# Optimization experiments

Measured on AMD Instinct MI355X. Metric: run time of the kernel, lower is better.

## Reference

```python
import jax, jax.numpy as jnp
import numpy as np

N_GENE = 4762
N_CELL = 847


def _graph_conv(x_src, src, dst, n_src, n_dst, W, b):
    """DGL GraphConv with norm='both': D_src^{-1/2} A D_dst^{-1/2} X W + b."""
    ones_e = jnp.ones(src.shape, jnp.float32)
    deg_out = jax.ops.segment_sum(ones_e, src, num_segments=n_src)
    norm_src = jnp.clip(deg_out, 1.0, None) ** -0.5
    feat = x_src * norm_src[:, None]            # [n_src, d]
    msg = feat[src]                              # gather  [E, d]
    agg = jax.ops.segment_sum(msg, dst, num_segments=n_dst)  # scatter-add [n_dst, d]
    deg_in = jax.ops.segment_sum(ones_e, dst, num_segments=n_dst)
    norm_dst = jnp.clip(deg_in, 1.0, None) ** -0.5
    return (agg * norm_dst[:, None]) @ W + b


def setup_inputs() -> dict:
    key = jax.random.key(0)
    ks = jax.random.split(key, 12)
    E = 200000
    d = 256
    inp = {
        "gene_emb": jax.random.normal(ks[0], (N_GENE, d), jnp.float32),
        "cell_emb": jax.random.normal(ks[1], (N_CELL, d), jnp.float32),
        "W_g2c": jax.random.normal(ks[2], (d, d), jnp.float32) * (1.0 / np.sqrt(d)),
        "b_g2c": jnp.zeros((d,), jnp.float32),
        "W_c2g": jax.random.normal(ks[3], (d, d), jnp.float32) * (1.0 / np.sqrt(d)),
        "b_c2g": jnp.zeros((d,), jnp.float32),
        "Wp": jax.random.normal(ks[4], (2 * d, 1), jnp.float32) * (1.0 / np.sqrt(2 * d)),
        "bp": jnp.zeros((1,), jnp.float32),
        "g2c_src": jax.random.randint(ks[5], (E,), 0, N_GENE, jnp.int32),
        "g2c_dst": jax.random.randint(ks[6], (E,), 0, N_CELL, jnp.int32),
        "c2g_src": jax.random.randint(ks[7], (E,), 0, N_CELL, jnp.int32),
        "c2g_dst": jax.random.randint(ks[8], (E,), 0, N_GENE, jnp.int32),
        "dec_src": jax.random.randint(ks[9], (E,), 0, N_GENE, jnp.int32),
        "dec_dst": jax.random.randint(ks[10], (E,), 0, N_CELL, jnp.int32),
    }
    return inp


def reference(gene_emb, cell_emb, W_g2c, b_g2c, W_c2g, b_c2g, Wp, bp,
              g2c_src, g2c_dst, c2g_src, c2g_dst, dec_src, dec_dst):
    # HeteroGraphConv (aggregate='sum'): each dst type receives from one relation here.
    h_cell = _graph_conv(gene_emb, g2c_src, g2c_dst, N_GENE, N_CELL, W_g2c, b_g2c)
    h_gene = _graph_conv(cell_emb, c2g_src, c2g_dst, N_CELL, N_GENE, W_c2g, b_c2g)
    h_gene = jax.nn.relu(h_gene)
    h_cell = jax.nn.relu(h_cell)
    # HeteroMLPPredictor: concat(src_h, dst_h) @ Wp + bp on dec_graph edges.
    x = jnp.concatenate([h_gene[dec_src], h_cell[dec_dst]], axis=1)  # [E_dec, 512]
    score = x @ Wp + bp                                               # [E_dec, 1]
    return (score, h_gene, h_cell)
```

## Files before the change

kernel.cpp:

```cpp
#include <hip/hip_runtime.h>

#define N_GENE 4762
#define N_CELL 847
#define NEDGE  200000
#define D      256
#define NPART  64

typedef __attribute__((ext_vector_type(8))) short short8;
typedef __attribute__((ext_vector_type(8))) unsigned short ushort8v;
typedef __attribute__((ext_vector_type(4))) float f32x4;

#define S_G_OUT 0
#define S_C_IN  (S_G_OUT + N_GENE)
#define S_C_OUT (S_C_IN + N_CELL)
#define S_G_IN  (S_C_OUT + N_CELL)
#define NBINS   (S_G_IN + N_GENE)

#define ALIGN8(x) (((x) + 7) & ~7)

#define A_DEG      0
#define A_NRM      (A_DEG + NBINS)
#define A_OFFS_C   (A_NRM + NBINS)
#define A_OFFS_G   (A_OFFS_C + N_CELL + 1)
#define A_SORT_C   ALIGN8(A_OFFS_G + N_GENE + 1)
#define A_SORT_G   (A_SORT_C + 2 * NEDGE)
#define A_PART     (A_SORT_G + 2 * NEDGE)
#define A_SG       (A_PART + NPART * NBINS)
#define A_SC       (A_SG + N_GENE)
#define A_GENE_BF  ALIGN8(A_SC + N_CELL)
#define A_CELL_BF  ALIGN8(A_GENE_BF + N_GENE * D / 2)
#define A_WT1_BF   ALIGN8(A_CELL_BF + N_CELL * D / 2)
#define A_WT2_BF   ALIGN8(A_WT1_BF + D * D / 2)
#define A_AGGC_BF  ALIGN8(A_WT2_BF + D * D / 2)
#define A_AGGG_BF  ALIGN8(A_AGGC_BF + N_CELL * D / 2)

__device__ __forceinline__ unsigned short f2bf(float f) {
    unsigned u = __float_as_uint(f);
    u = (u + 0x7FFFu + ((u >> 16) & 1u)) >> 16;
    return (unsigned short)u;
}
__device__ __forceinline__ float bf2f(unsigned short b) {
    return __uint_as_float(((unsigned)b) << 16);
}

__global__ __launch_bounds__(1024) void k_pre(
        const int* __restrict__ g2c_src, const int* __restrict__ g2c_dst,
        const int* __restrict__ c2g_src, const int* __restrict__ c2g_dst,
        const float* __restrict__ gene_emb, const float* __restrict__ cell_emb,
        const float* __restrict__ W_g2c, const float* __restrict__ W_c2g,
        int* __restrict__ partial,
        unsigned short* __restrict__ gene_bf, unsigned short* __restrict__ cell_bf,
        unsigned short* __restrict__ wt1, unsigned short* __restrict__ wt2) {
    __shared__ int sh[NBINS];
    int B = blockIdx.x, T = threadIdx.x;
    if (B < NPART) {
        for (int j = T; j < NBINS; j += 1024) sh[j] = 0;
        __syncthreads();
        const int chunk = (NEDGE + NPART - 1) / NPART;
        int e0 = B * chunk, e1 = min(NEDGE, e0 + chunk);
        for (int e = e0 + T; e < e1; e += 1024) {
            atomicAdd(&sh[S_G_OUT + g2c_src[e]], 1);
            atomicAdd(&sh[S_C_IN  + g2c_dst[e]], 1);
            atomicAdd(&sh[S_C_OUT + c2g_src[e]], 1);
            atomicAdd(&sh[S_G_IN  + c2g_dst[e]], 1);
        }
        __syncthreads();
        int* pp = partial + B * NBINS;
        for (int j = T; j < NBINS; j += 1024) pp[j] = sh[j];
    } else {
        const int NG = N_GENE * D, NC = N_CELL * D, NW = D * D;
        const int total = NG + NC + 2 * NW;
        for (int i = (B - NPART) * 1024 + T; i < total; i += NPART * 1024) {
            if (i < NG) {
                gene_bf[i] = f2bf(gene_emb[i]);
            } else if (i < NG + NC) {
                int j = i - NG;
                cell_bf[j] = f2bf(cell_emb[j]);
            } else if (i < NG + NC + NW) {
                int j = i - NG - NC;
                wt1[j] = f2bf(W_g2c[(j & 255) * D + (j >> 8)]);
            } else {
                int j = i - NG - NC - NW;
                wt2[j] = f2bf(W_c2g[(j & 255) * D + (j >> 8)]);
            }
        }
    }
}

__global__ void k_reduce(int* __restrict__ partial, int* __restrict__ deg,
                         float* __restrict__ nrm) {
    int j = blockIdx.x * blockDim.x + threadIdx.x;
    if (j < NBINS) {
        int s = 0;
        #pragma unroll
        for (int b0 = 0; b0 < NPART; b0 += 32) {
            int t[32];
            #pragma unroll
            for (int u = 0; u < 32; u++) t[u] = partial[(b0 + u) * NBINS + j];
            #pragma unroll
            for (int u = 0; u < 32; u++) { partial[(b0 + u) * NBINS + j] = s; s += t[u]; }
        }
        deg[j] = s;
        nrm[j] = rsqrtf(fmaxf((float)s, 1.0f));
    }
}

__global__ __launch_bounds__(1024) void k_scatter(
        const int* __restrict__ g2c_src, const int* __restrict__ g2c_dst,
        const int* __restrict__ c2g_src, const int* __restrict__ c2g_dst,
        const int* __restrict__ deg, const int* __restrict__ partial,
        const float* __restrict__ nrm,
        int* __restrict__ offsC, int* __restrict__ offsG,
        int2* __restrict__ sortC, int2* __restrict__ sortG) {
    __shared__ int soffs[N_GENE + 1];
    __shared__ int scur[N_GENE];
    __shared__ int wsum[16];
    int T = threadIdx.x, blk = blockIdx.x, dir = blockIdx.y;
    const int* src  = dir ? c2g_src : g2c_src;
    const int* dst  = dir ? c2g_dst : g2c_dst;
    const int* dgs  = dir ? deg + S_G_IN : deg + S_C_IN;
    const float* nsv = dir ? nrm + S_C_OUT : nrm + S_G_OUT;
    int seg         = dir ? S_G_IN : S_C_IN;
    int nb          = dir ? N_GENE : N_CELL;
    int* goffs      = dir ? offsG : offsC;
    int2* sorted    = dir ? sortG : sortC;
    int per = (nb + 1023) >> 10;
    int i0 = T * per, i1 = min(nb, i0 + per);
    int loc[5];
    int s = 0;
    for (int i = i0; i < i1; i++) { loc[i - i0] = s; s += dgs[i]; }
    int lane = T & 63, w = T >> 6;
    int t = s;
    #pragma unroll
    for (int off = 1; off < 64; off <<= 1) {
        int u = __shfl_up(t, off);
        if (lane >= off) t += u;
    }
    if (lane == 63) wsum[w] = t;
    __syncthreads();
    if (w == 0 && lane < 16) {
        int x = wsum[lane];
        #pragma unroll
        for (int off = 1; off < 16; off <<= 1) {
            int u = __shfl_up(x, off);
            if (lane >= off) x += u;
        }
        wsum[lane] = x;
    }
    __syncthreads();
    int wbase = w ? wsum[w - 1] : 0;
    int excl = wbase + t - s;
    for (int i = i0; i < i1; i++) soffs[i] = excl + loc[i - i0];
    if (T == 1023) soffs[nb] = excl + s;
    __syncthreads();
    if (blk == 0)
        for (int j = T; j <= nb; j += 1024) goffs[j] = soffs[j];
    const int* basep = partial + blk * NBINS + seg;
    for (int j = T; j < nb; j += 1024) scur[j] = soffs[j] + basep[j];
    __syncthreads();
    const int chunk = (NEDGE + NPART - 1) / NPART;
    int e0 = blk * chunk, e1 = min(NEDGE, e0 + chunk);
    for (int e = e0 + T; e < e1; e += 1024) {
        int d = dst[e], sv = src[e];
        float nv = nsv[sv];
        int pos = atomicAdd(&scur[d], 1);
        sorted[pos] = make_int2(sv, __float_as_int(nv));
    }
}

__global__ __launch_bounds__(256) void k_agg(
        const unsigned short* __restrict__ gene_bf,
        const unsigned short* __restrict__ cell_bf,
        const int2* __restrict__ sortC, const int2* __restrict__ sortG,
        const int* __restrict__ offsC, const int* __restrict__ offsG,
        const float* __restrict__ nrm,
        unsigned short* __restrict__ aggC, unsigned short* __restrict__ aggG) {
    __shared__ int   sidx[4][64];
    __shared__ float snrm[4][64];
    __shared__ float pacc[4][256];
    int w = threadIdx.x >> 6, lane = threadIdx.x & 63;
    int half = lane >> 5, li = lane & 31;
    int B = blockIdx.x;
    bool isCell = B < N_CELL;

    int e0, e1;
    const unsigned short* emb;
    const int2* sorted;
    int node;
    if (isCell) {
        node = B;
        int f0 = offsC[node], f1 = offsC[node + 1];
        int ne = f1 - f0, nw = (ne + 3) >> 2;
        e0 = f0 + w * nw; e1 = min(f1, e0 + nw);
        emb = gene_bf; sorted = sortC;
    } else {
        node = (B - N_CELL) * 4 + w;
        if (node >= N_GENE) return;
        e0 = offsG[node]; e1 = offsG[node + 1];
        emb = cell_bf; sorted = sortG;
    }

    float acc[8];
    #pragma unroll
    for (int c = 0; c < 8; c++) acc[c] = 0.f;

    for (int base = e0; base < e1; base += 64) {
        int n = min(64, e1 - base);
        if (lane < n) {
            int2 pr = sorted[base + lane];
            sidx[w][lane] = pr.x;
            snrm[w][lane] = __int_as_float(pr.y);
        }
        int i = 0;
        for (; 2 * i + 8 <= n; i += 4) {
            int j0 = 2 * i + half, j1 = 2 * i + 2 + half;
            int j2 = 2 * i + 4 + half, j3 = 2 * i + 6 + half;
            ushort8v v0 = *(const ushort8v*)&emb[sidx[w][j0] * D + li * 8];
            ushort8v v1 = *(const ushort8v*)&emb[sidx[w][j1] * D + li * 8];
            ushort8v v2 = *(const ushort8v*)&emb[sidx[w][j2] * D + li * 8];
            ushort8v v3 = *(const ushort8v*)&emb[sidx[w][j3] * D + li * 8];
            float n0 = snrm[w][j0], n1 = snrm[w][j1];
            float n2 = snrm[w][j2], n3 = snrm[w][j3];
            #pragma unroll
            for (int c = 0; c < 8; c++)
                acc[c] += bf2f(v0[c]) * n0 + bf2f(v1[c]) * n1 +
                          bf2f(v2[c]) * n2 + bf2f(v3[c]) * n3;
        }
        int npair = (n + 1) >> 1;
        for (; i < npair; i++) {
            int jj = 2 * i + half;
            bool ok = jj < n;
            int idx = ok ? sidx[w][jj] : sidx[w][0];
            float nv = ok ? snrm[w][jj] : 0.f;
            ushort8v v = *(const ushort8v*)&emb[idx * D + li * 8];
            #pragma unroll
            for (int c = 0; c < 8; c++) acc[c] += bf2f(v[c]) * nv;
        }
    }
    #pragma unroll
    for (int c = 0; c < 8; c++) acc[c] += __shfl_xor(acc[c], 32);

    if (isCell) {
        if (half == 0) {
            #pragma unroll
            for (int c = 0; c < 8; c++) pacc[w][li * 8 + c] = acc[c];
        }
        __syncthreads();
        int T = threadIdx.x;
        float s2 = pacc[0][T] + pacc[1][T] + pacc[2][T] + pacc[3][T];
        aggC[node * D + T] = f2bf(s2 * nrm[S_C_IN + node]);
    } else {
        if (half == 0) {
            float ndv = nrm[S_G_IN + node];
            ushort8v o;
            #pragma unroll
            for (int c = 0; c < 8; c++) o[c] = f2bf(acc[c] * ndv);
            *(ushort8v*)&aggG[node * D + li * 8] = o;
        }
    }
}

__global__ __launch_bounds__(256) void k_gemm2(
        const unsigned short* __restrict__ aggC, const unsigned short* __restrict__ aggG,
        const unsigned short* __restrict__ wt1, const unsigned short* __restrict__ wt2,
        const float* __restrict__ b_g2c, const float* __restrict__ b_c2g,
        const float* __restrict__ Wp,
        float* __restrict__ hC, float* __restrict__ hG,
        float* __restrict__ sg, float* __restrict__ sc) {
    const int CT = (N_CELL + 15) / 16;
    const int GT = (N_GENE + 15) / 16;
    int wid = blockIdx.x * 4 + (threadIdx.x >> 6);
    if (wid >= CT + GT) return;
    bool isCell = wid < CT;
    int tile = isCell ? wid : wid - CT;
    int m0 = tile * 16;
    int M = isCell ? N_CELL : N_GENE;
    const unsigned short* A  = isCell ? aggC : aggG;
    const unsigned short* Wt = isCell ? wt1 : wt2;
    const float* bias = isCell ? b_g2c : b_c2g;
    const float* wp   = isCell ? Wp + D : Wp;
    float* H  = isCell ? hC : hG;
    float* sv = isCell ? sc : sg;
    int lane = threadIdx.x & 63;
    int l15 = lane & 15, quad = lane >> 4;
    int arow = m0 + l15;
    if (arow >= M) arow = M - 1;
    f32x4 acc[16];
    #pragma unroll
    for (int t = 0; t < 16; t++) acc[t] = (f32x4){0.f, 0.f, 0.f, 0.f};
    #pragma unroll
    for (int k0 = 0; k0 < D; k0 += 32) {
        short8 a = *(const short8*)&A[arow * D + k0 + quad * 8];
        #pragma unroll
        for (int t = 0; t < 16; t++) {
            short8 b = *(const short8*)&Wt[(t * 16 + l15) * D + k0 + quad * 8];
            acc[t] = __builtin_amdgcn_mfma_f32_16x16x32_bf16(a, b, acc[t], 0, 0, 0);
        }
    }
    float dot[4] = {0.f, 0.f, 0.f, 0.f};
    #pragma unroll
    for (int t = 0; t < 16; t++) {
        int col = t * 16 + l15;
        float bv = bias[col], wv = wp[col];
        #pragma unroll
        for (int r = 0; r < 4; r++) {
            int row = m0 + quad * 4 + r;
            float h = fmaxf(acc[t][r] + bv, 0.f);
            if (row < M) H[row * D + col] = h;
            dot[r] += h * wv;
        }
    }
    #pragma unroll
    for (int off = 1; off < 16; off <<= 1) {
        #pragma unroll
        for (int r = 0; r < 4; r++) dot[r] += __shfl_xor(dot[r], off);
    }
    if (l15 == 0) {
        #pragma unroll
        for (int r = 0; r < 4; r++) {
            int row = m0 + quad * 4 + r;
            if (row < M) sv[row] = dot[r];
        }
    }
}

__global__ void k_score(const int* __restrict__ dsrc, const int* __restrict__ ddst,
                        const float* __restrict__ sg, const float* __restrict__ sc,
                        const float* __restrict__ bp, float* __restrict__ out) {
    int i = blockIdx.x * blockDim.x + threadIdx.x;
    if (i < NEDGE) out[i] = sg[dsrc[i]] + sc[ddst[i]] + bp[0];
}

extern "C" void kernel_launch(void* const* d_in, const int* in_sizes, int n_in,
                              void* d_out, int out_size, void* d_ws, size_t ws_size,
                              hipStream_t stream) {
    const float* gene_emb = (const float*)d_in[0];
    const float* cell_emb = (const float*)d_in[1];
    const float* W_g2c    = (const float*)d_in[2];
    const float* b_g2c    = (const float*)d_in[3];
    const float* W_c2g    = (const float*)d_in[4];
    const float* b_c2g    = (const float*)d_in[5];
    const float* Wp       = (const float*)d_in[6];
    const float* bp       = (const float*)d_in[7];
    const int* g2c_src = (const int*)d_in[8];
    const int* g2c_dst = (const int*)d_in[9];
    const int* c2g_src = (const int*)d_in[10];
    const int* c2g_dst = (const int*)d_in[11];
    const int* dec_src = (const int*)d_in[12];
    const int* dec_dst = (const int*)d_in[13];

    int*   wsi = (int*)d_ws;
    float* wsf = (float*)d_ws;
    unsigned short* gene_bf = (unsigned short*)(wsi + A_GENE_BF);
    unsigned short* cell_bf = (unsigned short*)(wsi + A_CELL_BF);
    unsigned short* wt1     = (unsigned short*)(wsi + A_WT1_BF);
    unsigned short* wt2     = (unsigned short*)(wsi + A_WT2_BF);
    unsigned short* aggC    = (unsigned short*)(wsi + A_AGGC_BF);
    unsigned short* aggG    = (unsigned short*)(wsi + A_AGGG_BF);
    int2* sortC = (int2*)(wsi + A_SORT_C);
    int2* sortG = (int2*)(wsi + A_SORT_G);

    float* out = (float*)d_out;
    float* out_score = out;
    float* out_hgene = out + NEDGE;
    float* out_hcell = out + NEDGE + N_GENE * D;

    k_pre<<<2 * NPART, 1024, 0, stream>>>(g2c_src, g2c_dst, c2g_src, c2g_dst,
                                          gene_emb, cell_emb, W_g2c, W_c2g,
                                          wsi + A_PART, gene_bf, cell_bf, wt1, wt2);
    k_reduce<<<(NBINS + 255) / 256, 256, 0, stream>>>(wsi + A_PART, wsi + A_DEG,
                                                      wsf + A_NRM);
    {
        dim3 grid(NPART, 2);
        k_scatter<<<grid, 1024, 0, stream>>>(g2c_src, g2c_dst, c2g_src, c2g_dst,
                                             wsi + A_DEG, wsi + A_PART, wsf + A_NRM,
                                             wsi + A_OFFS_C, wsi + A_OFFS_G,
                                             sortC, sortG);
    }
    k_agg<<<N_CELL + (N_GENE + 3) / 4, 256, 0, stream>>>(
        gene_bf, cell_bf, sortC, sortG, wsi + A_OFFS_C, wsi + A_OFFS_G,
        wsf + A_NRM, aggC, aggG);
    {
        const int CT = (N_CELL + 15) / 16, GT = (N_GENE + 15) / 16;
        k_gemm2<<<(CT + GT + 3) / 4, 256, 0, stream>>>(aggC, aggG, wt1, wt2,
                                                       b_g2c, b_c2g, Wp,
                                                       out_hcell, out_hgene,
                                                       wsf + A_SG, wsf + A_SC);
    }
    k_score<<<(NEDGE + 255) / 256, 256, 0, stream>>>(dec_src, dec_dst,
                                                     wsf + A_SG, wsf + A_SC, bp, out_score);
}
```

Measured before the change: 159.3 us.

## Fold degree reduction into scatter kernel and vectorize bf16 conversion

Removes the separate k_reduce launch. Each scatter block now recomputes degree totals, source norms and its per-block base offsets directly from a transposed partial-histogram layout, and k_agg derives the destination norm from the CSR offsets. The embedding-to-bf16 conversion is vectorized to float4 loads and ushort4 stores. This saves one kernel launch and a global round trip, but every one of the 128 scatter blocks redundantly reads the full partial histogram, adding memory traffic and latency inside the scatter.

```diff
diff --git a/kernel.cpp b/kernel.cpp
--- a/kernel.cpp
+++ b/kernel.cpp
@@ -18,14 +18,12 @@
 
 #define ALIGN8(x) (((x) + 7) & ~7)
 
-#define A_DEG      0
-#define A_NRM      (A_DEG + NBINS)
-#define A_OFFS_C   (A_NRM + NBINS)
+#define A_OFFS_C   0
 #define A_OFFS_G   (A_OFFS_C + N_CELL + 1)
 #define A_SORT_C   ALIGN8(A_OFFS_G + N_GENE + 1)
 #define A_SORT_G   (A_SORT_C + 2 * NEDGE)
 #define A_PART     (A_SORT_G + 2 * NEDGE)
-#define A_SG       (A_PART + NPART * NBINS)
+#define A_SG       (A_PART + NBINS * NPART)
 #define A_SC       (A_SG + N_GENE)
 #define A_GENE_BF  ALIGN8(A_SC + N_CELL)
 #define A_CELL_BF  ALIGN8(A_GENE_BF + N_GENE * D / 2)
@@ -65,70 +63,78 @@
             atomicAdd(&sh[S_G_IN  + c2g_dst[e]], 1);
         }
         __syncthreads();
-        int* pp = partial + B * NBINS;
-        for (int j = T; j < NBINS; j += 1024) pp[j] = sh[j];
+        for (int j = T; j < NBINS; j += 1024) partial[j * NPART + B] = sh[j];
     } else {
-        const int NG = N_GENE * D, NC = N_CELL * D, NW = D * D;
-        const int total = NG + NC + 2 * NW;
+        const int NGv = N_GENE * D / 4, NCv = N_CELL * D / 4, NW = D * D;
+        const int total = NGv + NCv + 2 * NW;
         for (int i = (B - NPART) * 1024 + T; i < total; i += NPART * 1024) {
-            if (i < NG) {
-                gene_bf[i] = f2bf(gene_emb[i]);
-            } else if (i < NG + NC) {
-                int j = i - NG;
-                cell_bf[j] = f2bf(cell_emb[j]);
-            } else if (i < NG + NC + NW) {
-                int j = i - NG - NC;
+            if (i < NGv) {
+                float4 v = ((const float4*)gene_emb)[i];
+                ushort4 o = make_ushort4(f2bf(v.x), f2bf(v.y), f2bf(v.z), f2bf(v.w));
+                ((ushort4*)gene_bf)[i] = o;
+            } else if (i < NGv + NCv) {
+                int j = i - NGv;
+                float4 v = ((const float4*)cell_emb)[j];
+                ushort4 o = make_ushort4(f2bf(v.x), f2bf(v.y), f2bf(v.z), f2bf(v.w));
+                ((ushort4*)cell_bf)[j] = o;
+            } else if (i < NGv + NCv + NW) {
+                int j = i - NGv - NCv;
                 wt1[j] = f2bf(W_g2c[(j & 255) * D + (j >> 8)]);
             } else {
-                int j = i - NG - NC - NW;
+                int j = i - NGv - NCv - NW;
                 wt2[j] = f2bf(W_c2g[(j & 255) * D + (j >> 8)]);
             }
         }
-    }
-}
-
-__global__ void k_reduce(int* __restrict__ partial, int* __restrict__ deg,
-                         float* __restrict__ nrm) {
-    int j = blockIdx.x * blockDim.x + threadIdx.x;
-    if (j < NBINS) {
-        int s = 0;
-        #pragma unroll
-        for (int b0 = 0; b0 < NPART; b0 += 32) {
-            int t[32];
-            #pragma unroll
-            for (int u = 0; u < 32; u++) t[u] = partial[(b0 + u) * NBINS + j];
-            #pragma unroll
-            for (int u = 0; u < 32; u++) { partial[(b0 + u) * NBINS + j] = s; s += t[u]; }
-        }
-        deg[j] = s;
-        nrm[j] = rsqrtf(fmaxf((float)s, 1.0f));
     }
 }
 
 __global__ __launch_bounds__(1024) void k_scatter(
         const int* __restrict__ g2c_src, const int* __restrict__ g2c_dst,
         const int* __restrict__ c2g_src, const int* __restrict__ c2g_dst,
-        const int* __restrict__ deg, const int* __restrict__ partial,
-        const float* __restrict__ nrm,
+        const int* __restrict__ partial,
         int* __restrict__ offsC, int* __restrict__ offsG,
         int2* __restrict__ sortC, int2* __restrict__ sortG) {
-    __shared__ int soffs[N_GENE + 1];
-    __shared__ int scur[N_GENE];
-    __shared__ int wsum[16];
+    __shared__ int   soffs[N_GENE + 1];
+    __shared__ int   scur[N_GENE];
+    __shared__ float snrmL[N_GENE];
+    __shared__ int   wsum[16];
     int T = threadIdx.x, blk = blockIdx.x, dir = blockIdx.y;
     const int* src  = dir ? c2g_src : g2c_src;
     const int* dst  = dir ? c2g_dst : g2c_dst;
-    const int* dgs  = dir ? deg + S_G_IN : deg + S_C_IN;
-    const float* nsv = dir ? nrm + S_C_OUT : nrm + S_G_OUT;
-    int seg         = dir ? S_G_IN : S_C_IN;
-    int nb          = dir ? N_GENE : N_CELL;
+    int seg_dst     = dir ? S_G_IN : S_C_IN;
+    int seg_src     = dir ? S_C_OUT : S_G_OUT;
+    int nbd         = dir ? N_GENE : N_CELL;
+    int nbs         = dir ? N_CELL : N_GENE;
     int* goffs      = dir ? offsG : offsC;
     int2* sorted    = dir ? sortG : sortC;
-    int per = (nb + 1023) >> 10;
-    int i0 = T * per, i1 = min(nb, i0 + per);
-    int loc[5];
+
+    for (int j = T; j < nbs; j += 1024) {
+        const int4* pp = (const int4*)(partial + (seg_src + j) * NPART);
+        int tot = 0;
+        #pragma unroll
+        for (int q = 0; q < NPART / 4; q++) {
+            int4 v = pp[q];
+            tot += v.x + v.y + v.z + v.w;
+        }
+        snrmL[j] = rsqrtf(fmaxf((float)tot, 1.0f));
+    }
+    int per = (nbd + 1023) >> 10;
+    int i0 = T * per, i1 = min(nbd, i0 + per);
+    int loc[5], bl[5];
     int s = 0;
-    for (int i = i0; i < i1; i++) { loc[i - i0] = s; s += dgs[i]; }
+    for (int i = i0; i < i1; i++) {
+        const int* pp = partial + (seg_dst + i) * NPART;
+        int tot = 0, base = 0;
+        #pragma unroll
+        for (int b = 0; b < NPART; b++) {
+            int v = pp[b];
+            tot += v;
+            if (b < blk) base += v;
+        }
+        loc[i - i0] = s;
+        bl[i - i0] = base;
+        s += tot;
+    }
     int lane = T & 63, w = T >> 6;
     int t = s;
     #pragma unroll
@@ -150,19 +156,19 @@
     __syncthreads();
     int wbase = w ? wsum[w - 1] : 0;
     int excl = wbase + t - s;
-    for (int i = i0; i < i1; i++) soffs[i] = excl + loc[i - i0];
-    if (T == 1023) soffs[nb] = excl + s;
+    for (int i = i0; i < i1; i++) {
+        soffs[i] = excl + loc[i - i0];
+        scur[i]  = excl + loc[i - i0] + bl[i - i0];
+    }
+    if (T == 1023) soffs[nbd] = excl + s;
     __syncthreads();
     if (blk == 0)
-        for (int j = T; j <= nb; j += 1024) goffs[j] = soffs[j];
-    const int* basep = partial + blk * NBINS + seg;
-    for (int j = T; j < nb; j += 1024) scur[j] = soffs[j] + basep[j];
-    __syncthreads();
+        for (int j = T; j <= nbd; j += 1024) goffs[j] = soffs[j];
     const int chunk = (NEDGE + NPART - 1) / NPART;
     int e0 = blk * chunk, e1 = min(NEDGE, e0 + chunk);
     for (int e = e0 + T; e < e1; e += 1024) {
         int d = dst[e], sv = src[e];
-        float nv = nsv[sv];
+        float nv = snrmL[sv];
         int pos = atomicAdd(&scur[d], 1);
         sorted[pos] = make_int2(sv, __float_as_int(nv));
     }
@@ -173,7 +179,6 @@
         const unsigned short* __restrict__ cell_bf,
         const int2* __restrict__ sortC, const int2* __restrict__ sortG,
         const int* __restrict__ offsC, const int* __restrict__ offsG,
-        const float* __restrict__ nrm,
         unsigned short* __restrict__ aggC, unsigned short* __restrict__ aggG) {
     __shared__ int   sidx[4][64];
     __shared__ float snrm[4][64];
@@ -183,20 +188,22 @@
     int B = blockIdx.x;
     bool isCell = B < N_CELL;
 
-    int e0, e1;
+    int e0, e1, degv;
     const unsigned short* emb;
     const int2* sorted;
     int node;
     if (isCell) {
         node = B;
         int f0 = offsC[node], f1 = offsC[node + 1];
-        int ne = f1 - f0, nw = (ne + 3) >> 2;
+        degv = f1 - f0;
+        int nw = (degv + 3) >> 2;
         e0 = f0 + w * nw; e1 = min(f1, e0 + nw);
         emb = gene_bf; sorted = sortC;
     } else {
         node = (B - N_CELL) * 4 + w;
         if (node >= N_GENE) return;
         e0 = offsG[node]; e1 = offsG[node + 1];
+        degv = e1 - e0;
         emb = cell_bf; sorted = sortG;
     }
 
@@ -240,6 +247,7 @@
     #pragma unroll
     for (int c = 0; c < 8; c++) acc[c] += __shfl_xor(acc[c], 32);
 
+    float ndv = rsqrtf(fmaxf((float)degv, 1.0f));
     if (isCell) {
         if (half == 0) {
             #pragma unroll
@@ -248,10 +256,9 @@
         __syncthreads();
         int T = threadIdx.x;
         float s2 = pacc[0][T] + pacc[1][T] + pacc[2][T] + pacc[3][T];
-        aggC[node * D + T] = f2bf(s2 * nrm[S_C_IN + node]);
+        aggC[node * D + T] = f2bf(s2 * ndv);
     } else {
         if (half == 0) {
-            float ndv = nrm[S_G_IN + node];
             ushort8v o;
             #pragma unroll
             for (int c = 0; c < 8; c++) o[c] = f2bf(acc[c] * ndv);
@@ -368,18 +375,15 @@
     k_pre<<<2 * NPART, 1024, 0, stream>>>(g2c_src, g2c_dst, c2g_src, c2g_dst,
                                           gene_emb, cell_emb, W_g2c, W_c2g,
                                           wsi + A_PART, gene_bf, cell_bf, wt1, wt2);
-    k_reduce<<<(NBINS + 255) / 256, 256, 0, stream>>>(wsi + A_PART, wsi + A_DEG,
-                                                      wsf + A_NRM);
     {
         dim3 grid(NPART, 2);
         k_scatter<<<grid, 1024, 0, stream>>>(g2c_src, g2c_dst, c2g_src, c2g_dst,
-                                             wsi + A_DEG, wsi + A_PART, wsf + A_NRM,
+                                             wsi + A_PART,
                                              wsi + A_OFFS_C, wsi + A_OFFS_G,
                                              sortC, sortG);
     }
     k_agg<<<N_CELL + (N_GENE + 3) / 4, 256, 0, stream>>>(
-        gene_bf, cell_bf, sortC, sortG, wsi + A_OFFS_C, wsi + A_OFFS_G,
-        wsf + A_NRM, aggC, aggG);
+        gene_bf, cell_bf, sortC, sortG, wsi + A_OFFS_C, wsi + A_OFFS_G, aggC, aggG);
     {
         const int CT = (N_CELL + 15) / 16, GT = (N_GENE + 15) / 16;
         k_gemm2<<<(CT + GT + 3) / 4, 256, 0, stream>>>(aggC, aggG, wt1, wt2,
```

Result: slower. 196.1 us (+23.1%).

## Transpose degree partials to bin-major layout and vectorize embedding bf16 conversion

Applied to the files above, without the earlier changes.

Stores the per-block histogram partials with bins as the outer index, so the reduce kernel reads and writes each bin's 64 partials contiguously as int4 vectors instead of using strided loads. The scatter kernel now reads its per-block base with a stride of NPART. The embedding fp32 to bf16 conversion moves from one element per thread to float4 loads and ushort4 stores. The per-node norm load is hoisted earlier in the aggregation kernel. The price is strided writes in the histogram kernel and strided reads in the scatter kernel.

```diff
diff --git a/kernel.cpp b/kernel.cpp
--- a/kernel.cpp
+++ b/kernel.cpp
@@ -25,7 +25,7 @@
 #define A_SORT_C   ALIGN8(A_OFFS_G + N_GENE + 1)
 #define A_SORT_G   (A_SORT_C + 2 * NEDGE)
 #define A_PART     (A_SORT_G + 2 * NEDGE)
-#define A_SG       (A_PART + NPART * NBINS)
+#define A_SG       (A_PART + NBINS * NPART)
 #define A_SC       (A_SG + N_GENE)
 #define A_GENE_BF  ALIGN8(A_SC + N_CELL)
 #define A_CELL_BF  ALIGN8(A_GENE_BF + N_GENE * D / 2)
@@ -65,22 +65,25 @@
             atomicAdd(&sh[S_G_IN  + c2g_dst[e]], 1);
         }
         __syncthreads();
-        int* pp = partial + B * NBINS;
-        for (int j = T; j < NBINS; j += 1024) pp[j] = sh[j];
+        for (int j = T; j < NBINS; j += 1024) partial[j * NPART + B] = sh[j];
     } else {
-        const int NG = N_GENE * D, NC = N_CELL * D, NW = D * D;
-        const int total = NG + NC + 2 * NW;
+        const int NGv = N_GENE * D / 4, NCv = N_CELL * D / 4, NW = D * D;
+        const int total = NGv + NCv + 2 * NW;
         for (int i = (B - NPART) * 1024 + T; i < total; i += NPART * 1024) {
-            if (i < NG) {
-                gene_bf[i] = f2bf(gene_emb[i]);
-            } else if (i < NG + NC) {
-                int j = i - NG;
-                cell_bf[j] = f2bf(cell_emb[j]);
-            } else if (i < NG + NC + NW) {
-                int j = i - NG - NC;
+            if (i < NGv) {
+                float4 v = ((const float4*)gene_emb)[i];
+                ushort4 o = make_ushort4(f2bf(v.x), f2bf(v.y), f2bf(v.z), f2bf(v.w));
+                ((ushort4*)gene_bf)[i] = o;
+            } else if (i < NGv + NCv) {
+                int j = i - NGv;
+                float4 v = ((const float4*)cell_emb)[j];
+                ushort4 o = make_ushort4(f2bf(v.x), f2bf(v.y), f2bf(v.z), f2bf(v.w));
+                ((ushort4*)cell_bf)[j] = o;
+            } else if (i < NGv + NCv + NW) {
+                int j = i - NGv - NCv;
                 wt1[j] = f2bf(W_g2c[(j & 255) * D + (j >> 8)]);
             } else {
-                int j = i - NG - NC - NW;
+                int j = i - NGv - NCv - NW;
                 wt2[j] = f2bf(W_c2g[(j & 255) * D + (j >> 8)]);
             }
         }
@@ -91,14 +94,17 @@
                          float* __restrict__ nrm) {
     int j = blockIdx.x * blockDim.x + threadIdx.x;
     if (j < NBINS) {
+        int4* pp = (int4*)(partial + j * NPART);
         int s = 0;
         #pragma unroll
-        for (int b0 = 0; b0 < NPART; b0 += 32) {
-            int t[32];
-            #pragma unroll
-            for (int u = 0; u < 32; u++) t[u] = partial[(b0 + u) * NBINS + j];
-            #pragma unroll
-            for (int u = 0; u < 32; u++) { partial[(b0 + u) * NBINS + j] = s; s += t[u]; }
+        for (int q = 0; q < NPART / 4; q++) {
+            int4 v = pp[q];
+            int t0 = v.x, t1 = v.y, t2 = v.z, t3 = v.w;
+            v.x = s; s += t0;
+            v.y = s; s += t1;
+            v.z = s; s += t2;
+            v.w = s; s += t3;
+            pp[q] = v;
         }
         deg[j] = s;
         nrm[j] = rsqrtf(fmaxf((float)s, 1.0f));
@@ -155,8 +161,8 @@
     __syncthreads();
     if (blk == 0)
         for (int j = T; j <= nb; j += 1024) goffs[j] = soffs[j];
-    const int* basep = partial + blk * NBINS + seg;
-    for (int j = T; j < nb; j += 1024) scur[j] = soffs[j] + basep[j];
+    const int* basep = partial + seg * NPART + blk;
+    for (int j = T; j < nb; j += 1024) scur[j] = soffs[j] + basep[j * NPART];
     __syncthreads();
     const int chunk = (NEDGE + NPART - 1) / NPART;
     int e0 = blk * chunk, e1 = min(NEDGE, e0 + chunk);
@@ -187,17 +193,20 @@
     const unsigned short* emb;
     const int2* sorted;
     int node;
+    float ndv;
     if (isCell) {
         node = B;
         int f0 = offsC[node], f1 = offsC[node + 1];
-        int ne = f1 - f0, nw = (ne + 3) >> 2;
+        int nw = (f1 - f0 + 3) >> 2;
         e0 = f0 + w * nw; e1 = min(f1, e0 + nw);
         emb = gene_bf; sorted = sortC;
+        ndv = nrm[S_C_IN + node];
     } else {
         node = (B - N_CELL) * 4 + w;
         if (node >= N_GENE) return;
         e0 = offsG[node]; e1 = offsG[node + 1];
         emb = cell_bf; sorted = sortG;
+        ndv = nrm[S_G_IN + node];
     }
 
     float acc[8];
@@ -248,10 +257,9 @@
         __syncthreads();
         int T = threadIdx.x;
         float s2 = pacc[0][T] + pacc[1][T] + pacc[2][T] + pacc[3][T];
-        aggC[node * D + T] = f2bf(s2 * nrm[S_C_IN + node]);
+        aggC[node * D + T] = f2bf(s2 * ndv);
     } else {
         if (half == 0) {
-            float ndv = nrm[S_G_IN + node];
             ushort8v o;
             #pragma unroll
             for (int c = 0; c < 8; c++) o[c] = f2bf(acc[c] * ndv);
```

Measured after the change: 170.7 us. +7.1%, slower.
